# Performance work log

Hardware: AMD Instinct MI355X
Metric: run time of the kernel (lower is better)

## Reference

```python
import jax, jax.numpy as jnp
import numpy as np

LN_EPS = 1e-5


def setup_inputs() -> dict:
    key = jax.random.key(0)
    ks = jax.random.split(key, 6)
    B, T, D, K = 8, 2048, 1024, 5
    x = jax.random.normal(ks[0], (B, T, D), dtype=jnp.float32)
    W_in = jax.random.normal(ks[1], (2 * D, D), dtype=jnp.float32) * (1.0 / np.sqrt(D))
    conv_w = jax.random.normal(ks[2], (D, 1, K), dtype=jnp.float32) * (1.0 / np.sqrt(K))
    conv_b = jax.random.normal(ks[3], (D,), dtype=jnp.float32) * 0.1
    a_param = jax.random.normal(ks[4], (D,), dtype=jnp.float32)
    W_out = jax.random.normal(ks[5], (D, D), dtype=jnp.float32) * (1.0 / np.sqrt(D))
    ln_w = jnp.ones((D,), dtype=jnp.float32)
    ln_b = jnp.zeros((D,), dtype=jnp.float32)
    return {"x": x, "W_in": W_in, "conv_w": conv_w, "conv_b": conv_b,
            "a_param": a_param, "W_out": W_out, "ln_w": ln_w, "ln_b": ln_b}


def _forward(x, W_in, conv_w, conv_b, a_param, W_out, ln_w, ln_b):
    B, T, D = x.shape
    K = conv_w.shape[-1]
    # in_proj: Linear(D -> 2D), torch weight layout [out, in]
    proj = jnp.einsum('btd,ed->bte', x, W_in)  # [B,T,2D]
    gate, val = proj[..., :D], proj[..., D:]
    g = jax.nn.sigmoid(gate)                   # [B,T,D]
    # depthwise conv1d with 'same' padding (K//2 each side)
    v = jax.lax.conv_general_dilated(
        val.transpose(0, 2, 1),                # [B,D,T]
        conv_w,                                # [D,1,K]
        window_strides=(1,),
        padding=[(K // 2, K // 2)],
        feature_group_count=D,
        dimension_numbers=('NCH', 'OIH', 'NCH'))
    v = (v + conv_b[None, :, None]).transpose(0, 2, 1)  # [B,T,D]
    a = jnp.tanh(a_param)                      # [D]
    gv = g * v                                 # [B,T,D] fused input to scan

    def step(h, u):
        h = a * h + u
        return h, h

    h0 = jnp.zeros((B, D), dtype=x.dtype)
    _, y = jax.lax.scan(step, h0, gv.transpose(1, 0, 2))  # y: [T,B,D]
    y = y.transpose(1, 0, 2)
    res = x + jnp.einsum('btd,ed->bte', y, W_out)
    mu = jnp.mean(res, axis=-1, keepdims=True)
    var = jnp.mean(jnp.square(res - mu), axis=-1, keepdims=True)
    return (res - mu) * jax.lax.rsqrt(var + LN_EPS) * ln_w + ln_b


def reference(x, W_in, conv_w, conv_b, a_param, W_out, ln_w, ln_b):
    return _forward(x, W_in, conv_w, conv_b, a_param, W_out, ln_w, ln_b)
```

## Files before the change

### kernel.cpp

```cpp
#include <hip/hip_runtime.h>
#include <hip/hip_bf16.h>

typedef unsigned short u16;
typedef unsigned int u32;
typedef __attribute__((ext_vector_type(8))) short bfrag;
typedef __attribute__((ext_vector_type(4))) float facc;

#define B_  8
#define T_  2048
#define D_  1024
#define M_  16384
#define NC_ 32
#define L_  64

static constexpr size_t OFF_XHI   = 0;
static constexpr size_t OFF_XLO   = 33554432;
static constexpr size_t OFF_WIHI  = 67108864;
static constexpr size_t OFF_WILO  = 71303168;
static constexpr size_t OFF_WOHI  = 75497472;
static constexpr size_t OFF_WOLO  = 77594624;
static constexpr size_t OFF_ATANH = 79691776;
static constexpr size_t OFF_G     = 79695872;
static constexpr size_t OFF_VAL   = 146804736;
static constexpr size_t OFF_CARRY = 213913600;
static constexpr size_t OFF_CIN   = 214962176;

__device__ __forceinline__ u16 f2bf(float f) {
  u32 u = __float_as_uint(f);
  u = (u + 0x7FFFu + ((u >> 16) & 1u)) >> 16;
  return (u16)u;
}
__device__ __forceinline__ float bf2f(u16 h) { return __uint_as_float(((u32)h) << 16); }

__device__ __forceinline__ void gload16(const void* g, void* l) {
  __builtin_amdgcn_global_load_lds((const __attribute__((address_space(1))) u32*)g,
                                   (__attribute__((address_space(3))) u32*)l, 16, 0, 0);
}

__global__ void split_kernel(const float* __restrict__ in, u16* __restrict__ hi,
                             u16* __restrict__ lo, int n4) {
  int i = blockIdx.x * 256 + threadIdx.x;
  if (i >= n4) return;
  float4 v = ((const float4*)in)[i];
  ushort4 h, l;
  h.x = f2bf(v.x); l.x = f2bf(v.x - bf2f(h.x));
  h.y = f2bf(v.y); l.y = f2bf(v.y - bf2f(h.y));
  h.z = f2bf(v.z); l.z = f2bf(v.z - bf2f(h.z));
  h.w = f2bf(v.w); l.w = f2bf(v.w - bf2f(h.w));
  ((ushort4*)hi)[i] = h;
  ((ushort4*)lo)[i] = l;
}

__global__ void tanh_kernel(const float* __restrict__ a_param, float* __restrict__ at) {
  int d = blockIdx.x * 256 + threadIdx.x;
  if (d < D_) at[d] = tanhf(a_param[d]);
}

template <int MODE>
__global__ __launch_bounds__(256, 2) void gemm_bf16x3(
    const u16* __restrict__ Ahi, const u16* __restrict__ Alo,
    const u16* __restrict__ Bhi, const u16* __restrict__ Blo,
    float* __restrict__ out0, float* __restrict__ out1, const float* __restrict__ resx) {
  __shared__ __attribute__((aligned(16))) u16 ldsA[128 * 64];
  __shared__ __attribute__((aligned(16))) u16 ldsB[128 * 64];
  const int tid = threadIdx.x;
  const int lane = tid & 63;
  const int wid = tid >> 6;
  const int wrow = wid >> 1, wcol = wid & 1;
  const int row0 = blockIdx.y * 128;
  const int col0 = blockIdx.x * 128;
  const int g = lane >> 4, lr = lane & 15;

  int aoh[4], aol[4], boh[4], bol[4];
#pragma unroll
  for (int i = 0; i < 4; i++) {
    int ra = wrow * 64 + i * 16 + lr;
    aoh[i] = ra * 64 + ((g) ^ (ra & 7)) * 8;
    aol[i] = ra * 64 + ((4 + g) ^ (ra & 7)) * 8;
    int rb = wcol * 64 + i * 16 + lr;
    boh[i] = rb * 64 + ((g) ^ (rb & 7)) * 8;
    bol[i] = rb * 64 + ((4 + g) ^ (rb & 7)) * 8;
  }

  facc acc[4][4] = {};

  for (int kt = 0; kt < 1024 / 32; ++kt) {
    __syncthreads();
#pragma unroll
    for (int p = 0; p < 4; p++) {
      int idx = p * 256 + tid;
      int row = idx >> 3, u = idx & 7;
      int ulog = u ^ (row & 7);
      const u16* sa = ((ulog < 4) ? Ahi : Alo) + (size_t)(row0 + row) * 1024 + kt * 32 + (ulog & 3) * 8;
      gload16(sa, &ldsA[idx * 8]);
      const u16* sb = ((ulog < 4) ? Bhi : Blo) + (size_t)(col0 + row) * 1024 + kt * 32 + (ulog & 3) * 8;
      gload16(sb, &ldsB[idx * 8]);
    }
    __syncthreads();

    bfrag ah[4], al[4], bh[4], bl[4];
#pragma unroll
    for (int i = 0; i < 4; i++) {
      ah[i] = *(const bfrag*)&ldsA[aoh[i]];
      al[i] = *(const bfrag*)&ldsA[aol[i]];
      bh[i] = *(const bfrag*)&ldsB[boh[i]];
      bl[i] = *(const bfrag*)&ldsB[bol[i]];
    }
#pragma unroll
    for (int i = 0; i < 4; i++)
#pragma unroll
      for (int j = 0; j < 4; j++) {
        acc[i][j] = __builtin_amdgcn_mfma_f32_16x16x32_bf16(ah[i], bh[j], acc[i][j], 0, 0, 0);
        acc[i][j] = __builtin_amdgcn_mfma_f32_16x16x32_bf16(ah[i], bl[j], acc[i][j], 0, 0, 0);
        acc[i][j] = __builtin_amdgcn_mfma_f32_16x16x32_bf16(al[i], bh[j], acc[i][j], 0, 0, 0);
      }
  }

#pragma unroll
  for (int i = 0; i < 4; i++)
#pragma unroll
    for (int j = 0; j < 4; j++)
#pragma unroll
      for (int r = 0; r < 4; r++) {
        int m = row0 + wrow * 64 + i * 16 + g * 4 + r;
        int n = col0 + wcol * 64 + j * 16 + lr;
        float c = acc[i][j][r];
        if (MODE == 0) {
          if (n < D_) out0[(size_t)m * D_ + n] = 1.f / (1.f + expf(-c));
          else        out1[(size_t)m * D_ + (n - D_)] = c;
        } else {
          out0[(size_t)m * D_ + n] = c + resx[(size_t)m * D_ + n];
        }
      }
}

__global__ void convscan_kernel(const float* __restrict__ val, const float* __restrict__ gbuf,
                                const float* __restrict__ conv_w, const float* __restrict__ conv_b,
                                const float* __restrict__ at, float* __restrict__ y,
                                float* __restrict__ carry) {
  const int d = blockIdx.x * 256 + threadIdx.x;
  const int c = blockIdx.y;
  const int b = blockIdx.z;
  const int t0 = c * L_;
  float cw0 = conv_w[(size_t)d * 5 + 0], cw1 = conv_w[(size_t)d * 5 + 1],
        cw2 = conv_w[(size_t)d * 5 + 2], cw3 = conv_w[(size_t)d * 5 + 3],
        cw4 = conv_w[(size_t)d * 5 + 4];
  float cb = conv_b[d];
  float a = at[d];
  const size_t base = (size_t)b * T_ * D_ + d;
  float w0 = (t0 - 2 >= 0) ? val[base + (size_t)(t0 - 2) * D_] : 0.f;
  float w1 = (t0 - 1 >= 0) ? val[base + (size_t)(t0 - 1) * D_] : 0.f;
  float w2 = val[base + (size_t)t0 * D_];
  float w3 = val[base + (size_t)(t0 + 1) * D_];
  float h = 0.f;
  for (int tt = 0; tt < L_; ++tt) {
    int t = t0 + tt;
    float w4 = (t + 2 < T_) ? val[base + (size_t)(t + 2) * D_] : 0.f;
    float conv = fmaf(w0, cw0, fmaf(w1, cw1, fmaf(w2, cw2, fmaf(w3, cw3, fmaf(w4, cw4, cb)))));
    float gg = gbuf[base + (size_t)t * D_];
    h = fmaf(a, h, gg * conv);
    y[base + (size_t)t * D_] = h;
    w0 = w1; w1 = w2; w2 = w3; w3 = w4;
  }
  carry[((size_t)b * NC_ + c) * D_ + d] = h;
}

__global__ void carryfix_kernel(const float* __restrict__ carry, const float* __restrict__ at,
                                float* __restrict__ cin) {
  int idx = blockIdx.x * 256 + threadIdx.x;
  int b = idx >> 10, d = idx & 1023;
  float a = at[d];
  float p = a;
  p = p * p; p = p * p; p = p * p; p = p * p; p = p * p; p = p * p;
  float H = 0.f;
  for (int c = 0; c < NC_; ++c) {
    size_t o = ((size_t)b * NC_ + c) * D_ + d;
    cin[o] = H;
    H = fmaf(p, H, carry[o]);
  }
}

__global__ void yfix_kernel(const float* __restrict__ yl, const float* __restrict__ cin,
                            const float* __restrict__ at, u16* __restrict__ yhi,
                            u16* __restrict__ ylo) {
  int i4 = blockIdx.x * 256 + threadIdx.x;
  int d4 = i4 & 255;
  int row = i4 >> 8;
  int t = row & (T_ - 1);
  int b = row >> 11;
  int tt = t & (L_ - 1);
  int c = t >> 6;
  float4 y4 = ((const float4*)yl)[i4];
  float4 ci = ((const float4*)cin)[((size_t)b * NC_ + c) * 256 + d4];
  float4 av = ((const float4*)at)[d4];
  float e = (float)(tt + 1);
  float out[4];
  float ys[4] = {y4.x, y4.y, y4.z, y4.w};
  float cs[4] = {ci.x, ci.y, ci.z, ci.w};
  float as[4] = {av.x, av.y, av.z, av.w};
#pragma unroll
  for (int q = 0; q < 4; q++) {
    float a = as[q];
    float p = exp2f(log2f(fabsf(a)) * e);
    if (a < 0.f && ((tt + 1) & 1)) p = -p;
    out[q] = fmaf(p, cs[q], ys[q]);
  }
  ushort4 h, l;
  h.x = f2bf(out[0]); l.x = f2bf(out[0] - bf2f(h.x));
  h.y = f2bf(out[1]); l.y = f2bf(out[1] - bf2f(h.y));
  h.z = f2bf(out[2]); l.z = f2bf(out[2] - bf2f(h.z));
  h.w = f2bf(out[3]); l.w = f2bf(out[3] - bf2f(h.w));
  ((ushort4*)yhi)[i4] = h;
  ((ushort4*)ylo)[i4] = l;
}

__global__ void ln_kernel(const float* __restrict__ res, const float* __restrict__ lnw,
                          const float* __restrict__ lnb, float* __restrict__ out) {
  const int row = blockIdx.x;
  const int tid = threadIdx.x;
  float4 v = ((const float4*)res)[(size_t)row * 256 + tid];
  float s = v.x + v.y + v.z + v.w;
  float q = v.x * v.x + v.y * v.y + v.z * v.z + v.w * v.w;
#pragma unroll
  for (int m = 1; m < 64; m <<= 1) {
    s += __shfl_xor(s, m);
    q += __shfl_xor(q, m);
  }
  __shared__ float red[2][4];
  const int wid = tid >> 6, lane = tid & 63;
  if (lane == 0) { red[0][wid] = s; red[1][wid] = q; }
  __syncthreads();
  s = red[0][0] + red[0][1] + red[0][2] + red[0][3];
  q = red[1][0] + red[1][1] + red[1][2] + red[1][3];
  float mu = s * (1.f / D_);
  float var = fmaxf(q * (1.f / D_) - mu * mu, 0.f);
  float inv = rsqrtf(var + 1e-5f);
  float4 w = ((const float4*)lnw)[tid];
  float4 bb = ((const float4*)lnb)[tid];
  float4 o;
  o.x = (v.x - mu) * inv * w.x + bb.x;
  o.y = (v.y - mu) * inv * w.y + bb.y;
  o.z = (v.z - mu) * inv * w.z + bb.z;
  o.w = (v.w - mu) * inv * w.w + bb.w;
  ((float4*)out)[(size_t)row * 256 + tid] = o;
}

extern "C" void kernel_launch(void* const* d_in, const int* in_sizes, int n_in,
                              void* d_out, int out_size, void* d_ws, size_t ws_size,
                              hipStream_t stream) {
  const float* x       = (const float*)d_in[0];
  const float* W_in    = (const float*)d_in[1];
  const float* conv_w  = (const float*)d_in[2];
  const float* conv_b  = (const float*)d_in[3];
  const float* a_param = (const float*)d_in[4];
  const float* W_out   = (const float*)d_in[5];
  const float* ln_w    = (const float*)d_in[6];
  const float* ln_b    = (const float*)d_in[7];
  float* out = (float*)d_out;
  char* ws = (char*)d_ws;

  u16* xhi  = (u16*)(ws + OFF_XHI);
  u16* xlo  = (u16*)(ws + OFF_XLO);
  u16* wihi = (u16*)(ws + OFF_WIHI);
  u16* wilo = (u16*)(ws + OFF_WILO);
  u16* wohi = (u16*)(ws + OFF_WOHI);
  u16* wolo = (u16*)(ws + OFF_WOLO);
  float* at    = (float*)(ws + OFF_ATANH);
  float* gbuf  = (float*)(ws + OFF_G);
  float* valb  = (float*)(ws + OFF_VAL);
  float* carry = (float*)(ws + OFF_CARRY);
  float* cin   = (float*)(ws + OFF_CIN);
  float* ybuf = out;
  float* resb = out;
  u16* yhi = (u16*)(ws + OFF_G);
  u16* ylo = (u16*)(ws + OFF_G + 33554432);

  split_kernel<<<16384, 256, 0, stream>>>(x, xhi, xlo, 4194304);
  split_kernel<<<2048, 256, 0, stream>>>(W_in, wihi, wilo, 524288);
  split_kernel<<<1024, 256, 0, stream>>>(W_out, wohi, wolo, 262144);
  tanh_kernel<<<4, 256, 0, stream>>>(a_param, at);

  gemm_bf16x3<0><<<dim3(16, 128), 256, 0, stream>>>(xhi, xlo, wihi, wilo, gbuf, valb, nullptr);

  convscan_kernel<<<dim3(4, 32, 8), 256, 0, stream>>>(valb, gbuf, conv_w, conv_b, at, ybuf, carry);
  carryfix_kernel<<<32, 256, 0, stream>>>(carry, at, cin);
  yfix_kernel<<<16384, 256, 0, stream>>>(ybuf, cin, at, yhi, ylo);

  gemm_bf16x3<1><<<dim3(8, 128), 256, 0, stream>>>(yhi, ylo, wohi, wolo, resb, nullptr, x);

  ln_kernel<<<16384, 256, 0, stream>>>(resb, ln_w, ln_b, out);
}
```

Before: 560.8 us.

## Enlarge GEMM tiles to 256x256 with double-buffered LDS prefetch

Grows the bf16x3 GEMM block tile from 128x128 to 256x256 with 512 threads, giving each wave a 128x64 output region for more operand reuse per LDS load. The LDS is double-buffered so the global-to-LDS loads for the next k-step are issued while the current step's MFMAs run. Waves sync at barriers around each quarter of work and raise priority during the MFMA sections. The cost is 128KB of LDS and 128 accumulator registers per lane, which limits occupancy to about one block per CU and adds barrier overhead.

```diff
diff --git a/kernel.cpp b/kernel.cpp
--- a/kernel.cpp
+++ b/kernel.cpp
@@ -57,74 +57,89 @@
 }
 
 template <int MODE>
-__global__ __launch_bounds__(256, 2) void gemm_bf16x3(
+__global__ __launch_bounds__(512, 2) void gemm_bf16x3(
     const u16* __restrict__ Ahi, const u16* __restrict__ Alo,
     const u16* __restrict__ Bhi, const u16* __restrict__ Blo,
     float* __restrict__ out0, float* __restrict__ out1, const float* __restrict__ resx) {
-  __shared__ __attribute__((aligned(16))) u16 ldsA[128 * 64];
-  __shared__ __attribute__((aligned(16))) u16 ldsB[128 * 64];
+  __shared__ __attribute__((aligned(16))) u16 lds[4][256 * 64];
   const int tid = threadIdx.x;
   const int lane = tid & 63;
   const int wid = tid >> 6;
-  const int wrow = wid >> 1, wcol = wid & 1;
-  const int row0 = blockIdx.y * 128;
-  const int col0 = blockIdx.x * 128;
+  const int wrow = wid >> 2;
+  const int wcol = wid & 3;
+  const int row0 = blockIdx.y * 256;
+  const int col0 = blockIdx.x * 256;
   const int g = lane >> 4, lr = lane & 15;
 
-  int aoh[4], aol[4], boh[4], bol[4];
-#pragma unroll
-  for (int i = 0; i < 4; i++) {
-    int ra = wrow * 64 + i * 16 + lr;
-    aoh[i] = ra * 64 + ((g) ^ (ra & 7)) * 8;
-    aol[i] = ra * 64 + ((4 + g) ^ (ra & 7)) * 8;
-    int rb = wcol * 64 + i * 16 + lr;
-    boh[i] = rb * 64 + ((g) ^ (rb & 7)) * 8;
-    bol[i] = rb * 64 + ((4 + g) ^ (rb & 7)) * 8;
-  }
-
-  facc acc[4][4] = {};
-
-  for (int kt = 0; kt < 1024 / 32; ++kt) {
-    __syncthreads();
+  facc acc[8][4] = {};
+
+  auto STAGE = [&](int buf, int kt) {
 #pragma unroll
     for (int p = 0; p < 4; p++) {
-      int idx = p * 256 + tid;
+      int idx = p * 512 + tid;
       int row = idx >> 3, u = idx & 7;
       int ulog = u ^ (row & 7);
       const u16* sa = ((ulog < 4) ? Ahi : Alo) + (size_t)(row0 + row) * 1024 + kt * 32 + (ulog & 3) * 8;
-      gload16(sa, &ldsA[idx * 8]);
+      gload16(sa, &lds[buf * 2 + 0][idx * 8]);
       const u16* sb = ((ulog < 4) ? Bhi : Blo) + (size_t)(col0 + row) * 1024 + kt * 32 + (ulog & 3) * 8;
-      gload16(sb, &ldsB[idx * 8]);
+      gload16(sb, &lds[buf * 2 + 1][idx * 8]);
     }
-    __syncthreads();
-
-    bfrag ah[4], al[4], bh[4], bl[4];
-#pragma unroll
-    for (int i = 0; i < 4; i++) {
-      ah[i] = *(const bfrag*)&ldsA[aoh[i]];
-      al[i] = *(const bfrag*)&ldsA[aol[i]];
-      bh[i] = *(const bfrag*)&ldsB[boh[i]];
-      bl[i] = *(const bfrag*)&ldsB[bol[i]];
+  };
+
+  STAGE(0, 0);
+  __syncthreads();
+
+  for (int t = 0; t < 32; ++t) {
+    const int cb = t & 1;
+    if (t) {
+      asm volatile("s_waitcnt vmcnt(0)" ::: "memory");
+      __builtin_amdgcn_s_barrier();
     }
-#pragma unroll
-    for (int i = 0; i < 4; i++)
-#pragma unroll
-      for (int j = 0; j < 4; j++) {
-        acc[i][j] = __builtin_amdgcn_mfma_f32_16x16x32_bf16(ah[i], bh[j], acc[i][j], 0, 0, 0);
-        acc[i][j] = __builtin_amdgcn_mfma_f32_16x16x32_bf16(ah[i], bl[j], acc[i][j], 0, 0, 0);
-        acc[i][j] = __builtin_amdgcn_mfma_f32_16x16x32_bf16(al[i], bh[j], acc[i][j], 0, 0, 0);
+    if (t + 1 < 32) STAGE(cb ^ 1, t + 1);
+    const u16* LA = &lds[cb * 2 + 0][0];
+    const u16* LB = &lds[cb * 2 + 1][0];
+
+#pragma unroll
+    for (int q = 0; q < 4; ++q) {
+      const int mh = q >> 1, nh = q & 1;
+      bfrag ah[4], al[4], bh[2], bl[2];
+#pragma unroll
+      for (int i = 0; i < 4; ++i) {
+        int ra = wrow * 128 + mh * 64 + i * 16 + lr;
+        ah[i] = *(const bfrag*)&LA[ra * 64 + ((g ^ (ra & 7))) * 8];
+        al[i] = *(const bfrag*)&LA[ra * 64 + (((4 + g) ^ (ra & 7))) * 8];
       }
-  }
-
-#pragma unroll
-  for (int i = 0; i < 4; i++)
-#pragma unroll
-    for (int j = 0; j < 4; j++)
-#pragma unroll
-      for (int r = 0; r < 4; r++) {
-        int m = row0 + wrow * 64 + i * 16 + g * 4 + r;
-        int n = col0 + wcol * 64 + j * 16 + lr;
-        float c = acc[i][j][r];
+#pragma unroll
+      for (int j = 0; j < 2; ++j) {
+        int rb = wcol * 64 + nh * 32 + j * 16 + lr;
+        bh[j] = *(const bfrag*)&LB[rb * 64 + ((g ^ (rb & 7))) * 8];
+        bl[j] = *(const bfrag*)&LB[rb * 64 + (((4 + g) ^ (rb & 7))) * 8];
+      }
+      __builtin_amdgcn_s_barrier();
+      __builtin_amdgcn_s_setprio(1);
+#pragma unroll
+      for (int i = 0; i < 4; ++i)
+#pragma unroll
+        for (int j = 0; j < 2; ++j) {
+          facc& A = acc[mh * 4 + i][nh * 2 + j];
+          A = __builtin_amdgcn_mfma_f32_16x16x32_bf16(ah[i], bh[j], A, 0, 0, 0);
+          A = __builtin_amdgcn_mfma_f32_16x16x32_bf16(ah[i], bl[j], A, 0, 0, 0);
+          A = __builtin_amdgcn_mfma_f32_16x16x32_bf16(al[i], bh[j], A, 0, 0, 0);
+        }
+      __builtin_amdgcn_s_setprio(0);
+      __builtin_amdgcn_s_barrier();
+    }
+  }
+
+#pragma unroll
+  for (int mi = 0; mi < 8; ++mi)
+#pragma unroll
+    for (int nj = 0; nj < 4; ++nj)
+#pragma unroll
+      for (int r = 0; r < 4; ++r) {
+        int m = row0 + wrow * 128 + (mi >> 2) * 64 + (mi & 3) * 16 + g * 4 + r;
+        int n = col0 + wcol * 64 + (nj >> 1) * 32 + (nj & 1) * 16 + lr;
+        float c = acc[mi][nj][r];
         if (MODE == 0) {
           if (n < D_) out0[(size_t)m * D_ + n] = 1.f / (1.f + expf(-c));
           else        out1[(size_t)m * D_ + (n - D_)] = c;
@@ -280,13 +295,13 @@
   split_kernel<<<1024, 256, 0, stream>>>(W_out, wohi, wolo, 262144);
   tanh_kernel<<<4, 256, 0, stream>>>(a_param, at);
 
-  gemm_bf16x3<0><<<dim3(16, 128), 256, 0, stream>>>(xhi, xlo, wihi, wilo, gbuf, valb, nullptr);
+  gemm_bf16x3<0><<<dim3(8, 64), 512, 0, stream>>>(xhi, xlo, wihi, wilo, gbuf, valb, nullptr);
 
   convscan_kernel<<<dim3(4, 32, 8), 256, 0, stream>>>(valb, gbuf, conv_w, conv_b, at, ybuf, carry);
   carryfix_kernel<<<32, 256, 0, stream>>>(carry, at, cin);
   yfix_kernel<<<16384, 256, 0, stream>>>(ybuf, cin, at, yhi, ylo);
 
-  gemm_bf16x3<1><<<dim3(8, 128), 256, 0, stream>>>(yhi, ylo, wohi, wolo, resb, nullptr, x);
+  gemm_bf16x3<1><<<dim3(4, 64), 512, 0, stream>>>(yhi, ylo, wohi, wolo, resb, nullptr, x);
 
   ln_kernel<<<16384, 256, 0, stream>>>(resb, ln_w, ln_b, out);
 }
```

After: 563.3 us. About the same (+0.4%).
